# Kernel tuning notes

Measured on AMD Instinct MI355X. Metric: run time of the kernel, lower is better.

## Reference

```python
import jax, jax.numpy as jnp
import numpy as np

NUM_POINTS = 25
NUM_SUBSET = 3
GROUPS = 8
OUT_CH = 64
BN_EPS = 1e-5


def setup_inputs() -> dict:
    key = jax.random.key(0)
    k = jax.random.split(key, 4)
    x0 = jax.random.normal(k[0], (32, 64, 288, NUM_POINTS), dtype=jnp.float32)
    # learned per-group adjacency (init from A repeated over groups; here random positive)
    decoupled_A = jax.random.uniform(k[1], (NUM_SUBSET, GROUPS, NUM_POINTS, NUM_POINTS), dtype=jnp.float32)
    linear_weight = jax.random.normal(k[2], (64, OUT_CH * NUM_SUBSET), dtype=jnp.float32) * np.sqrt(0.5 / (OUT_CH * NUM_SUBSET)).astype(np.float32)
    linear_bias = jnp.full((1, OUT_CH * NUM_SUBSET, 1, 1), 1e-6, dtype=jnp.float32)
    bn0_weight = jnp.ones((OUT_CH * NUM_SUBSET,), dtype=jnp.float32)
    bn0_bias = jnp.zeros((OUT_CH * NUM_SUBSET,), dtype=jnp.float32)
    bn_weight = jnp.full((OUT_CH,), 1e-6, dtype=jnp.float32)
    bn_bias = jnp.zeros((OUT_CH,), dtype=jnp.float32)
    return {"x0": x0, "decoupled_A": decoupled_A, "linear_weight": linear_weight,
            "linear_bias": linear_bias, "bn0_weight": bn0_weight, "bn0_bias": bn0_bias,
            "bn_weight": bn_weight, "bn_bias": bn_bias}


def _bn(x, gamma, beta):
    # training-mode BatchNorm2d: batch statistics over (N, T, V) per channel
    mean = jnp.mean(x, axis=(0, 2, 3), keepdims=True)
    var = jnp.var(x, axis=(0, 2, 3), keepdims=True)
    xhat = (x - mean) * jax.lax.rsqrt(var + BN_EPS)
    return xhat * gamma.reshape(1, -1, 1, 1) + beta.reshape(1, -1, 1, 1)


def _norm_adj(A):
    # A: [k, c, v, v]; column-normalize each [v, v] matrix: A @ diag(1/(colsum+1e-3))
    d = jnp.sum(A, axis=2, keepdims=True)          # [k, c, 1, v] column sums
    return A / (d + 0.001)


def reference(x0, decoupled_A, linear_weight, linear_bias, bn0_weight, bn0_bias, bn_weight, bn_bias):
    # expand groups to out_channels (torch .repeat tiles)
    learn_adj = jnp.tile(decoupled_A, (1, OUT_CH // GROUPS, 1, 1))  # [3, out, v, v]
    normed_adj = _norm_adj(learn_adj)
    # pointwise projection to out*num_subset channels
    x = jnp.einsum('nctw,cd->ndtw', x0, linear_weight) + linear_bias
    x = _bn(x, bn0_weight, bn0_bias)
    n, kc, t, v = x.shape
    x = x.reshape(n, NUM_SUBSET, kc // NUM_SUBSET, t, v)
    # decoupled graph conv: per-subset, per-channel small matmul over joints
    y = jnp.einsum('nkctv,kcvw->nctw', x, normed_adj)
    y = _bn(y, bn_weight, bn_bias)
    return jax.nn.relu(y + x0)  # in_channels == out_channels -> identity residual
```

## Files before the change

kernel.cpp:

```cpp
#include <hip/hip_runtime.h>
#include <hip/hip_bf16.h>

#define P_     7200
#define CNT_A  57600.0f
#define CNT_B  28800.0f

typedef __attribute__((ext_vector_type(8))) short bf16x8_t;
typedef __attribute__((ext_vector_type(4))) float f32x4_t;

struct __attribute__((aligned(8))) bf16x4 { __hip_bfloat16 a, b, c, d; };

#define OFF_X0T   ((size_t)0)
#define OFF_ANT   ((size_t)29495296)
#define OFF_WBFP  ((size_t)29544448)
#define OFF_WBFS  ((size_t)29569024)
#define OFF_CS    ((size_t)29593600)
#define OFF_CONST ((size_t)29596160)
#define OFF_SS    ((size_t)29602560)
#define OFF_STATP ((size_t)29603072)
#define OFF_P1    ((size_t)29627648)

static __device__ __forceinline__ unsigned short f2bs(float f) {
  __hip_bfloat16 h = __float2bfloat16(f);
  return *reinterpret_cast<unsigned short*>(&h);
}

__global__ __launch_bounds__(256) void kTP_kernel(
    const float* __restrict__ x0, __hip_bfloat16* __restrict__ x0t,
    float* __restrict__ zbuf) {
  __shared__ float x0s[64][81];
  const int pb = blockIdx.x, n = blockIdx.y, tid = threadIdx.x;
  if (n == 0 && pb < 2)
    for (int i = tid; i < 4096; i += 256) zbuf[pb * 4096 + i] = 0.f;

  const size_t base = (size_t)n * 64 * P_ + pb * 240;
#pragma unroll 1
  for (int sc = 0; sc < 3; ++sc) {
    __syncthreads();
    for (int i = tid; i < 1280; i += 256) {
      int c = i / 20, q = i % 20;
      float4 u = *(const float4*)(x0 + base + (size_t)c * P_ + sc * 80 + q * 4);
      x0s[c][q * 4 + 0] = u.x; x0s[c][q * 4 + 1] = u.y;
      x0s[c][q * 4 + 2] = u.z; x0s[c][q * 4 + 3] = u.w;
    }
    __syncthreads();
    for (int i = tid; i < 640; i += 256) {
      int p = i >> 3, cb = (i & 7) * 8;
      unsigned w0 = (unsigned)f2bs(x0s[cb + 0][p]) | ((unsigned)f2bs(x0s[cb + 1][p]) << 16);
      unsigned w1 = (unsigned)f2bs(x0s[cb + 2][p]) | ((unsigned)f2bs(x0s[cb + 3][p]) << 16);
      unsigned w2 = (unsigned)f2bs(x0s[cb + 4][p]) | ((unsigned)f2bs(x0s[cb + 5][p]) << 16);
      unsigned w3 = (unsigned)f2bs(x0s[cb + 6][p]) | ((unsigned)f2bs(x0s[cb + 7][p]) << 16);
      uint4 pk = {w0, w1, w2, w3};
      *(uint4*)(x0t + ((size_t)n * P_ + pb * 240 + sc * 80 + p) * 64 + cb) = pk;
    }
  }
}

__global__ __launch_bounds__(256) void prepA_kernel(
    const float* __restrict__ A, const float* __restrict__ W,
    float* __restrict__ cs, __hip_bfloat16* __restrict__ ant,
    __hip_bfloat16* __restrict__ wbfp) {
  const int b = blockIdx.x, tid = threadIdx.x;
  if (b < 24) {
    __shared__ float aL[625];
    __shared__ float csL[25];
    for (int i = tid; i < 625; i += 256) aL[i] = A[b * 625 + i];
    __syncthreads();
    if (tid < 25) {
      float s = 0.f;
      for (int vv = 0; vv < 25; ++vv) s += aL[vv * 25 + tid];
      csL[tid] = s;
      cs[b * 25 + tid] = s;
    }
    __syncthreads();
    for (int i = tid; i < 1024; i += 256) {
      int w = i >> 5, vv = i & 31;
      float val = 0.f;
      if (w < 25 && vv < 25) val = aL[vv * 25 + w] / (csL[w] + 0.001f);
      ant[b * 1024 + i] = __float2bfloat16(val);
    }
  } else {
    const int d0 = (b - 24) * 16;
    for (int i = tid; i < 1024; i += 256) {
      int dloc = d0 + (i >> 6), c = i & 63;
      wbfp[dloc * 64 + c] = __float2bfloat16(W[c * 192 + dloc]);
    }
  }
}

__global__ __launch_bounds__(256) void statsA_kernel(
    const __hip_bfloat16* __restrict__ x0t, const __hip_bfloat16* __restrict__ wbfp,
    float* __restrict__ statp) {
  const int tid = threadIdx.x, wave = tid >> 6, lane = tid & 63;
  const int a = lane & 15, g = lane >> 4;
  const int wid = blockIdx.x * 4 + wave;
  f32x4_t sa[12], s2[12];
#pragma unroll
  for (int dt = 0; dt < 12; ++dt) { sa[dt] = (f32x4_t){0,0,0,0}; s2[dt] = (f32x4_t){0,0,0,0}; }
#pragma unroll 1
  for (int st = 0; st < 4; ++st) {
    int j = wid + st * 900;
    int col0 = j * 64;
    int n = col0 / P_;
    int poff = col0 - n * P_;
    const __hip_bfloat16* bp = x0t + (((size_t)n * P_ + poff + a) << 6) + g * 8;
    bf16x8_t b0 = *(const bf16x8_t*)bp;
    bf16x8_t b1 = *(const bf16x8_t*)(bp + 32);
#pragma unroll
    for (int dt = 0; dt < 12; ++dt) {
      const __hip_bfloat16* wp = wbfp + ((dt * 16 + a) << 6) + g * 8;
      bf16x8_t a0 = *(const bf16x8_t*)wp;
      bf16x8_t a1 = *(const bf16x8_t*)(wp + 32);
      f32x4_t d = (f32x4_t){0,0,0,0};
      d = __builtin_amdgcn_mfma_f32_16x16x32_bf16(a0, b0, d, 0, 0, 0);
      d = __builtin_amdgcn_mfma_f32_16x16x32_bf16(a1, b1, d, 0, 0, 0);
      sa[dt] += d;
      s2[dt] += d * d;
    }
  }
#pragma unroll
  for (int off = 1; off < 16; off <<= 1)
#pragma unroll
    for (int dt = 0; dt < 12; ++dt)
#pragma unroll
      for (int q = 0; q < 4; ++q) {
        sa[dt][q] += __shfl_xor(sa[dt][q], off, 64);
        s2[dt][q] += __shfl_xor(s2[dt][q], off, 64);
      }
  if (a == 0) {
    int slot = wid & 15;
#pragma unroll
    for (int dt = 0; dt < 12; ++dt)
#pragma unroll
      for (int q = 0; q < 4; ++q) {
        int d = dt * 16 + g * 4 + q;
        atomicAdd(&statp[slot * 384 + d], sa[dt][q]);
        atomicAdd(&statp[slot * 384 + 192 + d], s2[dt][q]);
      }
  }
}

__global__ __launch_bounds__(256) void prep12_kernel(
    const float* __restrict__ W, const float* __restrict__ statp,
    const float* __restrict__ cs, const float* __restrict__ g0,
    const float* __restrict__ b0, __hip_bfloat16* __restrict__ wbfs,
    float* __restrict__ constcw) {
  __shared__ float akL[192], bkL[192];
  const int b = blockIdx.x, tid = threadIdx.x;
  if (tid < 192) {
    float s = 0.f, s2 = 0.f;
    for (int sl = 0; sl < 16; ++sl) {
      s  += statp[sl * 384 + tid];
      s2 += statp[sl * 384 + 192 + tid];
    }
    float mean = s / CNT_A;
    float var = fmaxf(s2 / CNT_A - mean * mean, 0.f);
    float ak = g0[tid] * rsqrtf(var + 1e-5f);
    akL[tid] = ak;
    bkL[tid] = b0[tid] - mean * ak;
  }
  __syncthreads();
  if (b < 12) {
    const int d0 = b * 16;
    for (int i = tid; i < 1024; i += 256) {
      int dloc = d0 + (i >> 6), c = i & 63;
      wbfs[dloc * 64 + c] = __float2bfloat16(akL[dloc] * W[c * 192 + dloc]);
    }
  } else {
    for (int i = tid; i < 1600; i += 256) {
      int c = i / 25, w = i % 25;
      float s = 0.f;
#pragma unroll
      for (int k = 0; k < 3; ++k) {
        float cv = cs[(k * 8 + (c & 7)) * 25 + w];
        s += bkL[k * 64 + c] * cv / (cv + 0.001f);
      }
      constcw[i] = s;
    }
  }
}

__global__ __launch_bounds__(512, 4) void statsB_kernel(
    const __hip_bfloat16* __restrict__ x0t, const __hip_bfloat16* __restrict__ wbfs,
    const __hip_bfloat16* __restrict__ ant, const float* __restrict__ constcw,
    float* __restrict__ part1) {
  __shared__ __align__(16) char smem[2 * 29696 + 3200];
  __hip_bfloat16* cstb = (__hip_bfloat16*)(smem + 2 * 29696);
  const int n = blockIdx.y, tb = blockIdx.x;
  const int tid = threadIdx.x, wave = tid >> 6, lane = tid & 63;
  const int a = lane & 15, g = lane >> 4;
  const int idx = tb * 8 + wave;
  const int eff = idx < 36 ? idx : 35;
  const int pbase = eff * 200;
  const int nslot = (tb == 4) ? 4 : 8;

  bf16x8_t af[2][2];
#pragma unroll
  for (int vh = 0; vh < 2; ++vh) {
    const __hip_bfloat16* p = x0t + (((size_t)n * P_ + pbase + vh * 16 + a) << 6) + g * 8;
    af[vh][0] = *(const bf16x8_t*)p;
    af[vh][1] = *(const bf16x8_t*)(p + 32);
  }
  for (int i = tid; i < 1600; i += 512) cstb[i] = __float2bfloat16(constcw[i]);
  if (tid < 128)
    *(uint4*)(smem + (tid >> 6) * 29696 + (tid & 63) * 464 + 448) = (uint4){0, 0, 0, 0};
  __syncthreads();

  f32x4_t yacc[4][2];
#pragma unroll
  for (int pr = 0; pr < 4; ++pr) {
    const int c = wave + 8 * (2 * pr + (a >> 3));
#pragma unroll
    for (int wt = 0; wt < 2; ++wt)
#pragma unroll
      for (int q = 0; q < 4; ++q) {
        int w = wt * 16 + g * 4 + q;
        yacc[pr][wt][q] = (w < 25) ? __bfloat162float(cstb[c * 25 + w]) : 0.f;
      }
  }

#define PROJB(kk, buf)                                                        \
  {                                                                           \
    _Pragma("unroll")                                                         \
    for (int dt = 0; dt < 4; ++dt) {                                          \
      const int dloc = dt * 16 + a;                                           \
      const __hip_bfloat16* wp = wbfs + ((((kk) << 6) + dloc) << 6) + g * 8;  \
      bf16x8_t w0 = *(const bf16x8_t*)wp;                                     \
      bf16x8_t w1 = *(const bf16x8_t*)(wp + 32);                              \
      _Pragma("unroll")                                                       \
      for (int vh = 0; vh < 2; ++vh) {                                        \
        f32x4_t p = (f32x4_t){0.f, 0.f, 0.f, 0.f};                            \
        p = __builtin_amdgcn_mfma_f32_16x16x32_bf16(af[vh][0], w0, p, 0, 0, 0); \
        p = __builtin_amdgcn_mfma_f32_16x16x32_bf16(af[vh][1], w1, p, 0, 0, 0); \
        if (vh == 1) {                                                        \
          _Pragma("unroll")                                                   \
          for (int q = 0; q < 4; ++q)                                         \
            if (g * 4 + q >= 9) p[q] = 0.f;                                   \
        }                                                                     \
        if (vh == 0 || g < 3) {                                               \
          uint2 pk;                                                           \
          pk.x = (unsigned)f2bs(p[0]) | ((unsigned)f2bs(p[1]) << 16);         \
          pk.y = (unsigned)f2bs(p[2]) | ((unsigned)f2bs(p[3]) << 16);         \
          *(uint2*)((buf) + dloc * 464 + wave * 56 + vh * 32 + g * 8) = pk;   \
        }                                                                     \
      }                                                                       \
    }                                                                         \
  }

#define CONVB(kk, buf)                                                        \
  {                                                                           \
    const __hip_bfloat16* ap = ant + ((((kk) * 8 + wave) * 2 * 16 + a) * 32) + g * 8; \
    bf16x8_t afr0 = *(const bf16x8_t*)ap;                                     \
    bf16x8_t afr1 = *(const bf16x8_t*)(ap + 512);                             \
    _Pragma("unroll")                                                         \
    for (int pr = 0; pr < 4; ++pr) {                                          \
      const int cl = wave + 8 * (2 * pr + (a >> 3));                          \
      const char* bp = (buf) + cl * 464 + (a & 7) * 56 + g * 16;              \
      uint2 lo = *(const uint2*)bp;                                           \
      uint2 hi = *(const uint2*)(bp + 8);                                     \
      uint4 u4 = {lo.x, lo.y, hi.x, hi.y};                                    \
      bf16x8_t bf = *reinterpret_cast<bf16x8_t*>(&u4);                        \
      yacc[pr][0] = __builtin_amdgcn_mfma_f32_16x16x32_bf16(afr0, bf, yacc[pr][0], 0, 0, 0); \
      yacc[pr][1] = __builtin_amdgcn_mfma_f32_16x16x32_bf16(afr1, bf, yacc[pr][1], 0, 0, 0); \
    }                                                                         \
  }

  PROJB(0, smem);
  __syncthreads();
  CONVB(0, smem); PROJB(1, smem + 29696);
  __syncthreads();
  CONVB(1, smem + 29696); PROJB(2, smem);
  __syncthreads();
  CONVB(2, smem);

  const int slot = (n * 5 + tb) & 15;
  const bool valid = (a & 7) < nslot;
#pragma unroll
  for (int pr = 0; pr < 4; ++pr) {
    float s = 0.f, s2 = 0.f;
    if (valid) {
#pragma unroll
      for (int wt = 0; wt < 2; ++wt)
#pragma unroll
        for (int q = 0; q < 4; ++q) {
          int w = wt * 16 + g * 4 + q;
          if (w < 25) {
            float val = yacc[pr][wt][q];
            s += val; s2 += val * val;
          }
        }
    }
#pragma unroll
    for (int off : {1, 2, 4, 16, 32}) {
      s  += __shfl_xor(s, off, 64);
      s2 += __shfl_xor(s2, off, 64);
    }
    if ((lane & 55) == 0) {
      const int c = wave + 8 * (2 * pr + (a >> 3));
      atomicAdd(&part1[slot * 128 + c], s);
      atomicAdd(&part1[slot * 128 + 64 + c], s2);
    }
  }
}

__global__ void fin_kernel(const float* __restrict__ part1,
                           const float* __restrict__ g1,
                           const float* __restrict__ b1,
                           float* __restrict__ ss) {
  __shared__ float tmp[128];
  int t = threadIdx.x;
  float s = 0.f;
  for (int sl = 0; sl < 16; ++sl) s += part1[sl * 128 + t];
  tmp[t] = s;
  __syncthreads();
  if (t < 64) {
    float mean = tmp[t] / CNT_B;
    float var = fmaxf(tmp[64 + t] / CNT_B - mean * mean, 0.f);
    float sc = g1[t] * rsqrtf(var + 1e-5f);
    ss[t] = sc;
    ss[64 + t] = b1[t] - mean * sc;
  }
}

__global__ __launch_bounds__(512, 4) void fused_kernel(
    const __hip_bfloat16* __restrict__ x0t, const float* __restrict__ x0,
    const __hip_bfloat16* __restrict__ wbfs, const __hip_bfloat16* __restrict__ ant,
    const float* __restrict__ constcw, const float* __restrict__ ss,
    float* __restrict__ outp) {
  __shared__ __align__(16) char smem[29696 + 6400 + 512];
  float* cst = (float*)(smem + 29696);
  float* ssl = (float*)(smem + 29696 + 6400);
  const int n = blockIdx.y, tb = blockIdx.x;
  const int tid = threadIdx.x, wave = tid >> 6, lane = tid & 63;
  const int a = lane & 15, g = lane >> 4;
  const size_t obase = (size_t)n * 64 * P_ + tb * 200;

  bf16x8_t af[2][2];
#pragma unroll
  for (int vh = 0; vh < 2; ++vh) {
    const __hip_bfloat16* p = x0t +
        (((size_t)n * P_ + tb * 200 + wave * 25 + vh * 16 + a) << 6) + g * 8;
    af[vh][0] = *(const bf16x8_t*)p;
    af[vh][1] = *(const bf16x8_t*)(p + 32);
  }
  for (int i = tid; i < 1600; i += 512) cst[i] = constcw[i];
  if (tid < 128) ssl[tid] = ss[tid];
  if (tid < 64) *(uint4*)(smem + tid * 464 + 448) = (uint4){0, 0, 0, 0};
  __syncthreads();

  f32x4_t yacc[8][2];
#pragma unroll
  for (int ci = 0; ci < 8; ++ci) {
    const int c = wave + 8 * ci;
#pragma unroll
    for (int wt = 0; wt < 2; ++wt)
#pragma unroll
      for (int q = 0; q < 4; ++q) {
        int w = wt * 16 + g * 4 + q;
        yacc[ci][wt][q] = (w < 25) ? cst[c * 25 + w] : 0.f;
      }
  }

#pragma unroll 1
  for (int k = 0; k < 3; ++k) {
#pragma unroll
    for (int dt = 0; dt < 4; ++dt) {
      const int dloc = dt * 16 + a;
      const __hip_bfloat16* wp = wbfs + (((k << 6) + dloc) << 6) + g * 8;
      bf16x8_t w0 = *(const bf16x8_t*)wp;
      bf16x8_t w1 = *(const bf16x8_t*)(wp + 32);
#pragma unroll
      for (int vh = 0; vh < 2; ++vh) {
        f32x4_t p = (f32x4_t){0.f, 0.f, 0.f, 0.f};
        p = __builtin_amdgcn_mfma_f32_16x16x32_bf16(af[vh][0], w0, p, 0, 0, 0);
        p = __builtin_amdgcn_mfma_f32_16x16x32_bf16(af[vh][1], w1, p, 0, 0, 0);
        if (vh == 1) {
#pragma unroll
          for (int q = 0; q < 4; ++q)
            if (g * 4 + q >= 9) p[q] = 0.f;
        }
        if (vh == 0 || g < 3) {
          uint2 pk;
          pk.x = (unsigned)f2bs(p[0]) | ((unsigned)f2bs(p[1]) << 16);
          pk.y = (unsigned)f2bs(p[2]) | ((unsigned)f2bs(p[3]) << 16);
          *(uint2*)(smem + dloc * 464 + wave * 56 + vh * 32 + g * 8) = pk;
        }
      }
    }
    __syncthreads();
    const __hip_bfloat16* ap = ant + (((k * 8 + wave) * 2 * 16 + a) * 32) + g * 8;
    bf16x8_t afr0 = *(const bf16x8_t*)ap;
    bf16x8_t afr1 = *(const bf16x8_t*)(ap + 512);
#pragma unroll
    for (int ci = 0; ci < 8; ++ci) {
      const int c = wave + 8 * ci;
      const char* bp = smem + c * 464 + (a & 7) * 56 + g * 16;
      uint2 lo = *(const uint2*)bp;
      uint2 hi = *(const uint2*)(bp + 8);
      uint4 u4 = {lo.x, lo.y, hi.x, hi.y};
      bf16x8_t bf = *reinterpret_cast<bf16x8_t*>(&u4);
      yacc[ci][0] = __builtin_amdgcn_mfma_f32_16x16x32_bf16(afr0, bf, yacc[ci][0], 0, 0, 0);
      yacc[ci][1] = __builtin_amdgcn_mfma_f32_16x16x32_bf16(afr1, bf, yacc[ci][1], 0, 0, 0);
    }
    __syncthreads();
  }

#pragma unroll
  for (int ci = 0; ci < 8; ++ci) {
    const int c = wave + 8 * ci;
    if (a < 8) {
#pragma unroll
      for (int wt = 0; wt < 2; ++wt)
#pragma unroll
        for (int q = 0; q < 4; ++q) {
          int w = wt * 16 + g * 4 + q;
          if (w < 25)
            *(__hip_bfloat16*)(smem + c * 464 + (a * 25 + w) * 2) =
                __float2bfloat16(yacc[ci][wt][q]);
        }
    }
  }
  __syncthreads();

#pragma unroll 1
  for (int i = tid; i < 3200; i += 512) {
    int c = i / 50, q = i % 50;
    uint2 yv2 = *(const uint2*)(smem + c * 464 + q * 8);
    bf16x4 yv = *reinterpret_cast<bf16x4*>(&yv2);
    float4 xv = *(const float4*)(x0 + obase + (size_t)c * P_ + q * 4);
    float sc = ssl[c], sh = ssl[64 + c];
    float4 r;
    r.x = fmaxf(__bfloat162float(yv.a) * sc + sh + xv.x, 0.f);
    r.y = fmaxf(__bfloat162float(yv.b) * sc + sh + xv.y, 0.f);
    r.z = fmaxf(__bfloat162float(yv.c) * sc + sh + xv.z, 0.f);
    r.w = fmaxf(__bfloat162float(yv.d) * sc + sh + xv.w, 0.f);
    *(float4*)(outp + obase + (size_t)c * P_ + q * 4) = r;
  }
}

extern "C" void kernel_launch(void* const* d_in, const int* in_sizes, int n_in,
                              void* d_out, int out_size, void* d_ws,
                              size_t ws_size, hipStream_t stream) {
  const float* x0 = (const float*)d_in[0];
  const float* A  = (const float*)d_in[1];
  const float* W  = (const float*)d_in[2];
  const float* g0 = (const float*)d_in[4];
  const float* b0 = (const float*)d_in[5];
  const float* g1 = (const float*)d_in[6];
  const float* b1 = (const float*)d_in[7];
  float* out = (float*)d_out;
  char* ws = (char*)d_ws;

  __hip_bfloat16* x0t  = (__hip_bfloat16*)(ws + OFF_X0T);
  __hip_bfloat16* ant  = (__hip_bfloat16*)(ws + OFF_ANT);
  __hip_bfloat16* wbfp = (__hip_bfloat16*)(ws + OFF_WBFP);
  __hip_bfloat16* wbfs = (__hip_bfloat16*)(ws + OFF_WBFS);
  float* cs      = (float*)(ws + OFF_CS);
  float* constcw = (float*)(ws + OFF_CONST);
  float* ssbuf   = (float*)(ws + OFF_SS);
  float* statp   = (float*)(ws + OFF_STATP);
  float* part1   = (float*)(ws + OFF_P1);

  kTP_kernel<<<dim3(30, 32), 256, 0, stream>>>(x0, x0t, statp);
  prepA_kernel<<<36, 256, 0, stream>>>(A, W, cs, ant, wbfp);
  statsA_kernel<<<225, 256, 0, stream>>>(x0t, wbfp, statp);
  prep12_kernel<<<13, 256, 0, stream>>>(W, statp, cs, g0, b0, wbfs, constcw);
  statsB_kernel<<<dim3(5, 32), 512, 0, stream>>>(x0t, wbfs, ant, constcw, part1);
  fin_kernel<<<1, 128, 0, stream>>>(part1, g1, b1, ssbuf);
  fused_kernel<<<dim3(36, 32), 512, 0, stream>>>(x0t, x0, wbfs, ant, constcw, ssbuf, out);
}
```

Baseline: 124.7 us.

## Fold prep and BN-finalize kernels into neighbors and batch residual loads

Merges the adjacency-normalization and weight-transpose prep work into the transpose kernel's first batch row. Every block of the fused kernel now recomputes the final BatchNorm scale and shift from the partial sums, which removes two small kernel launches. The epilogue loop now issues all residual x0 loads up front into registers before combining, to increase memory-level parallelism. The costs are some redundant per-block reduction work and higher register pressure in the fused kernel.

```diff
diff --git a/kernel.cpp b/kernel.cpp
--- a/kernel.cpp
+++ b/kernel.cpp
@@ -16,7 +16,6 @@
 #define OFF_WBFS  ((size_t)29569024)
 #define OFF_CS    ((size_t)29593600)
 #define OFF_CONST ((size_t)29596160)
-#define OFF_SS    ((size_t)29602560)
 #define OFF_STATP ((size_t)29603072)
 #define OFF_P1    ((size_t)29627648)
 
@@ -26,12 +25,45 @@
 }
 
 __global__ __launch_bounds__(256) void kTP_kernel(
-    const float* __restrict__ x0, __hip_bfloat16* __restrict__ x0t,
-    float* __restrict__ zbuf) {
+    const float* __restrict__ x0, const float* __restrict__ A,
+    const float* __restrict__ W, __hip_bfloat16* __restrict__ x0t,
+    float* __restrict__ cs, __hip_bfloat16* __restrict__ ant,
+    __hip_bfloat16* __restrict__ wbfp, float* __restrict__ zbuf) {
   __shared__ float x0s[64][81];
   const int pb = blockIdx.x, n = blockIdx.y, tid = threadIdx.x;
-  if (n == 0 && pb < 2)
-    for (int i = tid; i < 4096; i += 256) zbuf[pb * 4096 + i] = 0.f;
+
+  if (n == 0) {
+    if (pb < 24) {
+      float* aL  = &x0s[0][0];
+      float* csL = aL + 640;
+      for (int i = tid; i < 625; i += 256) aL[i] = A[pb * 625 + i];
+      __syncthreads();
+      if (tid < 25) {
+        float s = 0.f;
+        for (int vv = 0; vv < 25; ++vv) s += aL[vv * 25 + tid];
+        csL[tid] = s;
+        cs[pb * 25 + tid] = s;
+      }
+      __syncthreads();
+      for (int i = tid; i < 1024; i += 256) {
+        int w = i >> 5, vv = i & 31;
+        float val = 0.f;
+        if (w < 25 && vv < 25) val = aL[vv * 25 + w] / (csL[w] + 0.001f);
+        ant[pb * 1024 + i] = __float2bfloat16(val);
+      }
+    } else {
+      const int b = pb - 24;
+      for (int i = tid; i < 2048; i += 256) {
+        int e = b * 2048 + i;
+        int dloc = e >> 6, c = e & 63;
+        wbfp[e] = __float2bfloat16(W[c * 192 + dloc]);
+      }
+      for (int i = tid; i < 1366; i += 256) {
+        int e = b * 1366 + i;
+        if (e < 8192) zbuf[e] = 0.f;
+      }
+    }
+  }
 
   const size_t base = (size_t)n * 64 * P_ + pb * 240;
 #pragma unroll 1
@@ -52,38 +84,6 @@
       unsigned w3 = (unsigned)f2bs(x0s[cb + 6][p]) | ((unsigned)f2bs(x0s[cb + 7][p]) << 16);
       uint4 pk = {w0, w1, w2, w3};
       *(uint4*)(x0t + ((size_t)n * P_ + pb * 240 + sc * 80 + p) * 64 + cb) = pk;
-    }
-  }
-}
-
-__global__ __launch_bounds__(256) void prepA_kernel(
-    const float* __restrict__ A, const float* __restrict__ W,
-    float* __restrict__ cs, __hip_bfloat16* __restrict__ ant,
-    __hip_bfloat16* __restrict__ wbfp) {
-  const int b = blockIdx.x, tid = threadIdx.x;
-  if (b < 24) {
-    __shared__ float aL[625];
-    __shared__ float csL[25];
-    for (int i = tid; i < 625; i += 256) aL[i] = A[b * 625 + i];
-    __syncthreads();
-    if (tid < 25) {
-      float s = 0.f;
-      for (int vv = 0; vv < 25; ++vv) s += aL[vv * 25 + tid];
-      csL[tid] = s;
-      cs[b * 25 + tid] = s;
-    }
-    __syncthreads();
-    for (int i = tid; i < 1024; i += 256) {
-      int w = i >> 5, vv = i & 31;
-      float val = 0.f;
-      if (w < 25 && vv < 25) val = aL[vv * 25 + w] / (csL[w] + 0.001f);
-      ant[b * 1024 + i] = __float2bfloat16(val);
-    }
-  } else {
-    const int d0 = (b - 24) * 16;
-    for (int i = tid; i < 1024; i += 256) {
-      int dloc = d0 + (i >> 6), c = i & 63;
-      wbfp[dloc * 64 + c] = __float2bfloat16(W[c * 192 + dloc]);
     }
   }
 }
@@ -303,29 +303,11 @@
   }
 }
 
-__global__ void fin_kernel(const float* __restrict__ part1,
-                           const float* __restrict__ g1,
-                           const float* __restrict__ b1,
-                           float* __restrict__ ss) {
-  __shared__ float tmp[128];
-  int t = threadIdx.x;
-  float s = 0.f;
-  for (int sl = 0; sl < 16; ++sl) s += part1[sl * 128 + t];
-  tmp[t] = s;
-  __syncthreads();
-  if (t < 64) {
-    float mean = tmp[t] / CNT_B;
-    float var = fmaxf(tmp[64 + t] / CNT_B - mean * mean, 0.f);
-    float sc = g1[t] * rsqrtf(var + 1e-5f);
-    ss[t] = sc;
-    ss[64 + t] = b1[t] - mean * sc;
-  }
-}
-
 __global__ __launch_bounds__(512, 4) void fused_kernel(
     const __hip_bfloat16* __restrict__ x0t, const float* __restrict__ x0,
     const __hip_bfloat16* __restrict__ wbfs, const __hip_bfloat16* __restrict__ ant,
-    const float* __restrict__ constcw, const float* __restrict__ ss,
+    const float* __restrict__ constcw, const float* __restrict__ part1,
+    const float* __restrict__ g1, const float* __restrict__ b1,
     float* __restrict__ outp) {
   __shared__ __align__(16) char smem[29696 + 6400 + 512];
   float* cst = (float*)(smem + 29696);
@@ -344,9 +326,22 @@
     af[vh][1] = *(const bf16x8_t*)(p + 32);
   }
   for (int i = tid; i < 1600; i += 512) cst[i] = constcw[i];
-  if (tid < 128) ssl[tid] = ss[tid];
+  if (tid < 128) {
+    float s = 0.f;
+#pragma unroll
+    for (int sl = 0; sl < 16; ++sl) s += part1[sl * 128 + tid];
+    ssl[tid] = s;
+  }
   if (tid < 64) *(uint4*)(smem + tid * 464 + 448) = (uint4){0, 0, 0, 0};
   __syncthreads();
+  if (tid < 64) {
+    float mean = ssl[tid] / CNT_B;
+    float var = fmaxf(ssl[64 + tid] / CNT_B - mean * mean, 0.f);
+    float sc = g1[tid] * rsqrtf(var + 1e-5f);
+    float sh = b1[tid] - mean * sc;
+    ssl[tid] = sc;
+    ssl[64 + tid] = sh;
+  }
 
   f32x4_t yacc[8][2];
 #pragma unroll
@@ -422,19 +417,30 @@
   }
   __syncthreads();
 
-#pragma unroll 1
-  for (int i = tid; i < 3200; i += 512) {
-    int c = i / 50, q = i % 50;
-    uint2 yv2 = *(const uint2*)(smem + c * 464 + q * 8);
-    bf16x4 yv = *reinterpret_cast<bf16x4*>(&yv2);
-    float4 xv = *(const float4*)(x0 + obase + (size_t)c * P_ + q * 4);
-    float sc = ssl[c], sh = ssl[64 + c];
-    float4 r;
-    r.x = fmaxf(__bfloat162float(yv.a) * sc + sh + xv.x, 0.f);
-    r.y = fmaxf(__bfloat162float(yv.b) * sc + sh + xv.y, 0.f);
-    r.z = fmaxf(__bfloat162float(yv.c) * sc + sh + xv.z, 0.f);
-    r.w = fmaxf(__bfloat162float(yv.d) * sc + sh + xv.w, 0.f);
-    *(float4*)(outp + obase + (size_t)c * P_ + q * 4) = r;
+  float4 xv[7];
+#pragma unroll
+  for (int j = 0; j < 7; ++j) {
+    const int i = tid + 512 * j;
+    if (j < 6 || i < 3200) {
+      int c = i / 50, q = i - c * 50;
+      xv[j] = *(const float4*)(x0 + obase + (size_t)c * P_ + q * 4);
+    }
+  }
+#pragma unroll
+  for (int j = 0; j < 7; ++j) {
+    const int i = tid + 512 * j;
+    if (j < 6 || i < 3200) {
+      int c = i / 50, q = i - c * 50;
+      uint2 yv2 = *(const uint2*)(smem + c * 464 + q * 8);
+      bf16x4 yv = *reinterpret_cast<bf16x4*>(&yv2);
+      float sc = ssl[c], sh = ssl[64 + c];
+      float4 r;
+      r.x = fmaxf(__bfloat162float(yv.a) * sc + sh + xv[j].x, 0.f);
+      r.y = fmaxf(__bfloat162float(yv.b) * sc + sh + xv[j].y, 0.f);
+      r.z = fmaxf(__bfloat162float(yv.c) * sc + sh + xv[j].z, 0.f);
+      r.w = fmaxf(__bfloat162float(yv.d) * sc + sh + xv[j].w, 0.f);
+      *(float4*)(outp + obase + (size_t)c * P_ + q * 4) = r;
+    }
   }
 }
 
@@ -457,15 +463,13 @@
   __hip_bfloat16* wbfs = (__hip_bfloat16*)(ws + OFF_WBFS);
   float* cs      = (float*)(ws + OFF_CS);
   float* constcw = (float*)(ws + OFF_CONST);
-  float* ssbuf   = (float*)(ws + OFF_SS);
   float* statp   = (float*)(ws + OFF_STATP);
   float* part1   = (float*)(ws + OFF_P1);
 
-  kTP_kernel<<<dim3(30, 32), 256, 0, stream>>>(x0, x0t, statp);
-  prepA_kernel<<<36, 256, 0, stream>>>(A, W, cs, ant, wbfp);
+  kTP_kernel<<<dim3(30, 32), 256, 0, stream>>>(x0, A, W, x0t, cs, ant, wbfp, statp);
   statsA_kernel<<<225, 256, 0, stream>>>(x0t, wbfp, statp);
   prep12_kernel<<<13, 256, 0, stream>>>(W, statp, cs, g0, b0, wbfs, constcw);
   statsB_kernel<<<dim3(5, 32), 512, 0, stream>>>(x0t, wbfs, ant, constcw, part1);
-  fin_kernel<<<1, 128, 0, stream>>>(part1, g1, b1, ssbuf);
-  fused_kernel<<<dim3(36, 32), 512, 0, stream>>>(x0t, x0, wbfs, ant, constcw, ssbuf, out);
-}
+  fused_kernel<<<dim3(36, 32), 512, 0, stream>>>(x0t, x0, wbfs, ant, constcw,
+                                                 part1, g1, b1, out);
+}
```

After: 122.9 us. About the same (-1.4%).
